# Kernel tuning notes

Hardware: AMD Instinct MI355X
Metric: run time of the kernel (lower is better)

The kernel has to match this reference:

```python
import jax, jax.numpy as jnp
import numpy as np

BINS = 10          # init kwarg `bins`
LOSS_WEIGHT = 1.0  # init kwarg `loss_weight`


def setup_inputs() -> dict:
    key = jax.random.key(0)
    k1, k2, k3 = jax.random.split(key, 3)
    B, C = 131072, 80  # [batch_num(anchors), class_num]
    pred = jax.random.normal(k1, (B, C), dtype=jnp.float32)
    target = jax.random.randint(k2, (B, C), 0, 2).astype(jnp.int32)
    label_weight = jax.random.randint(k3, (B, C), 0, 2).astype(jnp.int32)
    return {"pred": pred, "target": target, "label_weight": label_weight}


def _ghmc_loss(pred, target_f, valid_f):
    # total number of valid samples (>=1), matches max(valid.sum().item(), 1.0)
    total = jnp.maximum(valid_f.sum(), 1.0)

    # gradient magnitude g = |sigmoid(pred).detach() - target|, in [0, 1]
    g = jnp.abs(jax.nn.sigmoid(jax.lax.stop_gradient(pred)) - target_f)

    # bin index: edges are i/bins, last edge padded by 1e-6, so
    # floor(g * bins) clipped to [0, bins-1] reproduces the torch loop's
    # per-element assignment (elements exactly on an edge take the later bin,
    # matching the sequential overwrite of weights[inds]).
    bin_idx = jnp.clip(jnp.floor(g * BINS).astype(jnp.int32), 0, BINS - 1)

    # histogram of valid elements per bin (invalid routed to extra bin BINS)
    flat_idx = jnp.where(valid_f > 0, bin_idx, BINS).reshape(-1)
    counts = jnp.bincount(flat_idx, length=BINS + 1)[:BINS].astype(pred.dtype)

    # n = number of non-empty bins (>=1 whenever any element is valid)
    n = jnp.maximum((counts > 0).sum(), 1).astype(pred.dtype)

    # per-bin weight total/num_in_bin, zero for empty bins, then /n
    w_bin = jnp.where(counts > 0, total / jnp.maximum(counts, 1.0), 0.0) / n
    weights = jnp.where(valid_f > 0, w_bin[bin_idx], 0.0)
    weights = jax.lax.stop_gradient(weights)  # histogram weights are detached

    # weighted BCE-with-logits, reduction='sum', then / total
    bce = target_f * jax.nn.softplus(-pred) + (1.0 - target_f) * jax.nn.softplus(pred)
    return (weights * bce).sum() / total * LOSS_WEIGHT


def reference(pred, target, label_weight):
    target_f = target.astype(pred.dtype)
    valid_f = (label_weight > 0).astype(pred.dtype)
    return _ghmc_loss(pred, target_f, valid_f)
```

## Files before the change

### kernel.cpp

```cpp
#include <hip/hip_runtime.h>

#define BINS 10
#define TPB  256
#define NB_MAX 2048
#define FTPB 1024
#define KPACK 16384.0f
#define LN2f  0.69314718055994531f

__global__ __launch_bounds__(TPB, 4) void ghmc_hist_kernel(
    const float4* __restrict__ pred4,
    const int4*   __restrict__ tgt4,
    const int4*   __restrict__ lw4,
    float* __restrict__ part,
    int n4, int n)
{
    float acc[BINS];
#pragma unroll
    for (int b = 0; b < BINS; ++b) acc[b] = 0.f;

    auto proc = [&](float p, int t, int w) {
        float q     = __int_as_float(__float_as_int(p) ^ (t << 31));
        float e     = __builtin_amdgcn_exp2f(fabsf(q) * -1.44269504089f);
        float d     = 1.f + e;
        float r     = __builtin_amdgcn_rcpf(d);
        float num   = (q >= 0.f) ? 1.0f : e;
        float sig10 = num * (10.f * r);
        int bin     = (int)sig10;
        bin = bin < (BINS - 1) ? bin : (BINS - 1);
        float bce2  = fmaf(fmaxf(q, 0.f), 1.44269504089f,
                           __builtin_amdgcn_logf(d));
        int   vm    = 0 - (int)(w > 0);
        float v     = bce2 + KPACK;
        int   vbits = __float_as_int(v) & vm;
        int   bit   = 1 << bin;
#pragma unroll
        for (int b = 0; b < BINS; ++b) {
            int sel = __builtin_amdgcn_sbfe(bit, b, 1);
            acc[b] += __int_as_float(sel & vbits);
        }
    };

    const int tid    = threadIdx.x;
    const int stride = gridDim.x * TPB;
    const int base   = blockIdx.x * TPB + tid;
    const int full   = n4 / stride;

    int i = base;
    float4 pA; int4 tA, wA;
    if (full > 0) { pA = pred4[i]; tA = tgt4[i]; wA = lw4[i]; }
    for (int k = 0; k < full - 1; ++k) {
        const int j = i + stride;
        float4 pB = pred4[j]; int4 tB = tgt4[j]; int4 wB = lw4[j];
        proc(pA.x, tA.x, wA.x); proc(pA.y, tA.y, wA.y);
        proc(pA.z, tA.z, wA.z); proc(pA.w, tA.w, wA.w);
        pA = pB; tA = tB; wA = wB;
        i = j;
    }
    if (full > 0) {
        proc(pA.x, tA.x, wA.x); proc(pA.y, tA.y, wA.y);
        proc(pA.z, tA.z, wA.z); proc(pA.w, tA.w, wA.w);
    }
    {
        const int j = base + full * stride;
        if (j < n4) {
            float4 p = pred4[j]; int4 t = tgt4[j]; int4 w = lw4[j];
            proc(p.x, t.x, w.x); proc(p.y, t.y, w.y);
            proc(p.z, t.z, w.z); proc(p.w, t.w, w.w);
        }
    }
    if (blockIdx.x == 0 && tid < (n & 3)) {
        const float* predf = (const float*)pred4;
        const int*   tgtf  = (const int*)tgt4;
        const int*   lwf   = (const int*)lw4;
        const int j = n4 * 4 + tid;
        proc(predf[j], tgtf[j], lwf[j]);
    }

#pragma unroll
    for (int b = 0; b < BINS; ++b) {
#pragma unroll
        for (int off = 1; off <= 8; off <<= 1)
            acc[b] += __shfl_xor(acc[b], off, 64);
    }

    __shared__ float red[2 * BINS][16];
    const int grp = tid >> 4;
    if ((tid & 15) == 0) {
#pragma unroll
        for (int b = 0; b < BINS; ++b) {
            float Cf = floorf(acc[b] * (1.f / KPACK));
            red[b][grp]        = acc[b] - KPACK * Cf;
            red[BINS + b][grp] = Cf;
        }
    }
    __syncthreads();
    if (tid < 2 * BINS) {
        float v = 0.f;
#pragma unroll
        for (int g = 0; g < 16; ++g) v += red[tid][g];
        part[blockIdx.x * (2 * BINS) + tid] = v;
    }
}

__global__ __launch_bounds__(FTPB) void ghmc_final_kernel(
    const float* __restrict__ part, float* __restrict__ out, int nb)
{
    float acc[2 * BINS];
#pragma unroll
    for (int v = 0; v < 2 * BINS; ++v) acc[v] = 0.f;

    const int tid = threadIdx.x;
    for (int i = tid; i < nb; i += FTPB) {
        const float4* rec = (const float4*)(part + (size_t)i * (2 * BINS));
        float4 a = rec[0], b = rec[1], c = rec[2], d = rec[3], e = rec[4];
        acc[0]  += a.x; acc[1]  += a.y; acc[2]  += a.z; acc[3]  += a.w;
        acc[4]  += b.x; acc[5]  += b.y; acc[6]  += b.z; acc[7]  += b.w;
        acc[8]  += c.x; acc[9]  += c.y; acc[10] += c.z; acc[11] += c.w;
        acc[12] += d.x; acc[13] += d.y; acc[14] += d.z; acc[15] += d.w;
        acc[16] += e.x; acc[17] += e.y; acc[18] += e.z; acc[19] += e.w;
    }

#pragma unroll
    for (int v = 0; v < 2 * BINS; ++v) {
#pragma unroll
        for (int off = 1; off <= 32; off <<= 1)
            acc[v] += __shfl_xor(acc[v], off, 64);
    }

    __shared__ float sh[2 * BINS][16];
    const int wv = tid >> 6, lane = tid & 63;
    if (lane == 0) {
#pragma unroll
        for (int v = 0; v < 2 * BINS; ++v) sh[v][wv] = acc[v];
    }
    __syncthreads();
    if (tid < 2 * BINS) {
        float s = 0.f;
#pragma unroll
        for (int g = 0; g < 16; ++g) s += sh[tid][g];
        sh[tid][0] = s;
    }
    __syncthreads();

    if (tid == 0) {
        float ti = 0.f; int nbn = 0;
        float cnts[BINS];
#pragma unroll
        for (int b = 0; b < BINS; ++b) {
            cnts[b] = sh[BINS + b][0];
            ti += cnts[b];
            nbn += (cnts[b] > 0.f) ? 1 : 0;
        }
        float total = fmaxf(ti, 1.f);
        float nf    = (float)(nbn > 0 ? nbn : 1);
        float loss  = 0.f;
#pragma unroll
        for (int b = 0; b < BINS; ++b) {
            if (cnts[b] > 0.f) {
                float w = (total / cnts[b]) / nf;
                loss += w * (sh[b][0] * LN2f);
            }
        }
        out[0] = loss / total * 1.0f;
    }
}

extern "C" void kernel_launch(void* const* d_in, const int* in_sizes, int n_in,
                              void* d_out, int out_size, void* d_ws, size_t ws_size,
                              hipStream_t stream)
{
    const float4* pred4 = (const float4*)d_in[0];
    const int4*   tgt4  = (const int4*)d_in[1];
    const int4*   lw4   = (const int4*)d_in[2];

    const int n  = in_sizes[0];
    const int n4 = n / 4;

    int nb = (n4 + TPB - 1) / TPB;
    if (nb > NB_MAX) nb = NB_MAX;
    int ws_cap = (int)(ws_size / (2 * BINS * sizeof(float)));
    if (nb > ws_cap) nb = ws_cap;
    if (nb < 1) nb = 1;

    float* part = (float*)d_ws;

    ghmc_hist_kernel<<<nb, TPB, 0, stream>>>(pred4, tgt4, lw4, part, n4, n);
    ghmc_final_kernel<<<1, FTPB, 0, stream>>>(part, (float*)d_out, nb);
}
```

Before: 37.77 us.

## Stage inputs via async global-to-LDS double buffer and use logit-threshold cumulative bins

The input stream is now prefetched with global_load_lds into a two-slot LDS buffer, with explicit vmcnt waits, so the next tile's loads overlap compute on the current tile. Bin assignment no longer uses a sigmoid, rcp and one-hot bit extraction. Each element is compared against logit thresholds and added into cumulative bin accumulators, and the final kernel recovers per-bin counts and sums by differencing. This trades the rcp and bit select for 9 compare-selects, adds LDS traffic and hand-written waitcnt scheduling, and risks small mismatches at bin edges plus precision loss from subtracting cumulative sums.

```diff
diff --git a/kernel.cpp b/kernel.cpp
--- a/kernel.cpp
+++ b/kernel.cpp
@@ -5,7 +5,15 @@
 #define NB_MAX 2048
 #define FTPB 1024
 #define KPACK 16384.0f
-#define LN2f  0.69314718055994531f
+#define LN2f   0.69314718055994531f
+#define LOG2Ef 1.44269504088896f
+
+template <typename T>
+__device__ __forceinline__ void gload16(const T* g, T* l) {
+    __builtin_amdgcn_global_load_lds(
+        (const __attribute__((address_space(1))) void*)g,
+        (__attribute__((address_space(3))) void*)l, 16, 0, 0);
+}
 
 __global__ __launch_bounds__(TPB, 4) void ghmc_hist_kernel(
     const float4* __restrict__ pred4,
@@ -14,30 +22,30 @@
     float* __restrict__ part,
     int n4, int n)
 {
-    float acc[BINS];
-#pragma unroll
-    for (int b = 0; b < BINS; ++b) acc[b] = 0.f;
+    __shared__ float4 Lp[2][TPB];
+    __shared__ int4   Lt[2][TPB];
+    __shared__ int4   Lw[2][TPB];
+    __shared__ float  red[2 * BINS][16];
+
+    float A[BINS];
+#pragma unroll
+    for (int b = 0; b < BINS; ++b) A[b] = 0.f;
+
+    const float Q[9] = {-2.19722458f, -1.38629436f, -0.84729786f,
+                        -0.40546511f,  0.0f,         0.40546511f,
+                         0.84729786f,  1.38629436f,  2.19722458f};
 
     auto proc = [&](float p, int t, int w) {
-        float q     = __int_as_float(__float_as_int(p) ^ (t << 31));
-        float e     = __builtin_amdgcn_exp2f(fabsf(q) * -1.44269504089f);
-        float d     = 1.f + e;
-        float r     = __builtin_amdgcn_rcpf(d);
-        float num   = (q >= 0.f) ? 1.0f : e;
-        float sig10 = num * (10.f * r);
-        int bin     = (int)sig10;
-        bin = bin < (BINS - 1) ? bin : (BINS - 1);
-        float bce2  = fmaf(fmaxf(q, 0.f), 1.44269504089f,
-                           __builtin_amdgcn_logf(d));
-        int   vm    = 0 - (int)(w > 0);
-        float v     = bce2 + KPACK;
-        int   vbits = __float_as_int(v) & vm;
-        int   bit   = 1 << bin;
-#pragma unroll
-        for (int b = 0; b < BINS; ++b) {
-            int sel = __builtin_amdgcn_sbfe(bit, b, 1);
-            acc[b] += __int_as_float(sel & vbits);
-        }
+        float q    = __int_as_float(__float_as_int(p) ^ (int)((unsigned)t << 31));
+        float e    = __builtin_amdgcn_exp2f(fabsf(q) * -LOG2Ef);
+        float d    = 1.f + e;
+        float bce2 = fmaf(fmaxf(q, 0.f), LOG2Ef,
+                          __builtin_amdgcn_logf(d));
+        float v    = (w > 0) ? (bce2 + KPACK) : 0.f;
+        A[0] += v;
+#pragma unroll
+        for (int k = 0; k < 9; ++k)
+            A[k + 1] += (q >= Q[k]) ? v : 0.f;
     };
 
     const int tid    = threadIdx.x;
@@ -45,20 +53,49 @@
     const int base   = blockIdx.x * TPB + tid;
     const int full   = n4 / stride;
 
-    int i = base;
-    float4 pA; int4 tA, wA;
-    if (full > 0) { pA = pred4[i]; tA = tgt4[i]; wA = lw4[i]; }
-    for (int k = 0; k < full - 1; ++k) {
-        const int j = i + stride;
-        float4 pB = pred4[j]; int4 tB = tgt4[j]; int4 wB = lw4[j];
-        proc(pA.x, tA.x, wA.x); proc(pA.y, tA.y, wA.y);
-        proc(pA.z, tA.z, wA.z); proc(pA.w, tA.w, wA.w);
-        pA = pB; tA = tB; wA = wB;
-        i = j;
-    }
-    if (full > 0) {
-        proc(pA.x, tA.x, wA.x); proc(pA.y, tA.y, wA.y);
-        proc(pA.z, tA.z, wA.z); proc(pA.w, tA.w, wA.w);
+    if (full >= 2) {
+        gload16(&pred4[base],          &Lp[0][tid]);
+        gload16(&tgt4 [base],          &Lt[0][tid]);
+        gload16(&lw4  [base],          &Lw[0][tid]);
+        gload16(&pred4[base + stride], &Lp[1][tid]);
+        gload16(&tgt4 [base + stride], &Lt[1][tid]);
+        gload16(&lw4  [base + stride], &Lw[1][tid]);
+
+        for (int k = 0; k < full - 1; ++k) {
+            asm volatile("s_waitcnt vmcnt(3)" ::: "memory");
+            __builtin_amdgcn_sched_barrier(0);
+            const int b2 = k & 1;
+            float4 p = Lp[b2][tid];
+            int4   t = Lt[b2][tid];
+            int4   w = Lw[b2][tid];
+            asm volatile("s_waitcnt lgkmcnt(0)" ::: "memory");
+            __builtin_amdgcn_sched_barrier(0);
+            if (k + 2 < full) {
+                const int j = base + (k + 2) * stride;
+                gload16(&pred4[j], &Lp[b2][tid]);
+                gload16(&tgt4 [j], &Lt[b2][tid]);
+                gload16(&lw4  [j], &Lw[b2][tid]);
+            }
+            proc(p.x, t.x, w.x); proc(p.y, t.y, w.y);
+            proc(p.z, t.z, w.z); proc(p.w, t.w, w.w);
+        }
+        {
+            asm volatile("s_waitcnt vmcnt(0)" ::: "memory");
+            __builtin_amdgcn_sched_barrier(0);
+            const int b2 = (full - 1) & 1;
+            float4 p = Lp[b2][tid];
+            int4   t = Lt[b2][tid];
+            int4   w = Lw[b2][tid];
+            proc(p.x, t.x, w.x); proc(p.y, t.y, w.y);
+            proc(p.z, t.z, w.z); proc(p.w, t.w, w.w);
+        }
+    } else {
+        for (int k = 0; k < full; ++k) {
+            const int j = base + k * stride;
+            float4 p = pred4[j]; int4 t = tgt4[j]; int4 w = lw4[j];
+            proc(p.x, t.x, w.x); proc(p.y, t.y, w.y);
+            proc(p.z, t.z, w.z); proc(p.w, t.w, w.w);
+        }
     }
     {
         const int j = base + full * stride;
@@ -80,16 +117,15 @@
     for (int b = 0; b < BINS; ++b) {
 #pragma unroll
         for (int off = 1; off <= 8; off <<= 1)
-            acc[b] += __shfl_xor(acc[b], off, 64);
-    }
-
-    __shared__ float red[2 * BINS][16];
+            A[b] += __shfl_xor(A[b], off, 64);
+    }
+
     const int grp = tid >> 4;
     if ((tid & 15) == 0) {
 #pragma unroll
         for (int b = 0; b < BINS; ++b) {
-            float Cf = floorf(acc[b] * (1.f / KPACK));
-            red[b][grp]        = acc[b] - KPACK * Cf;
+            float Cf = floorf(A[b] * (1.f / KPACK));
+            red[b][grp]        = A[b] - KPACK * Cf;
             red[BINS + b][grp] = Cf;
         }
     }
@@ -143,22 +179,28 @@
     __syncthreads();
 
     if (tid == 0) {
-        float ti = 0.f; int nbn = 0;
-        float cnts[BINS];
+        float PS2[BINS + 1], PC[BINS + 1];
+        PS2[BINS] = 0.f; PC[BINS] = 0.f;
+#pragma unroll
+        for (int b = 0; b < BINS; ++b) { PS2[b] = sh[b][0]; PC[b] = sh[BINS + b][0]; }
+
+        float ti = PC[0];
+        int nbn = 0;
+        float cnts[BINS], sums[BINS];
 #pragma unroll
         for (int b = 0; b < BINS; ++b) {
-            cnts[b] = sh[BINS + b][0];
-            ti += cnts[b];
-            nbn += (cnts[b] > 0.f) ? 1 : 0;
+            cnts[b] = PC[b]  - PC[b + 1];
+            sums[b] = PS2[b] - PS2[b + 1];
+            nbn += (cnts[b] > 0.5f) ? 1 : 0;
         }
         float total = fmaxf(ti, 1.f);
         float nf    = (float)(nbn > 0 ? nbn : 1);
         float loss  = 0.f;
 #pragma unroll
         for (int b = 0; b < BINS; ++b) {
-            if (cnts[b] > 0.f) {
+            if (cnts[b] > 0.5f) {
                 float w = (total / cnts[b]) / nf;
-                loss += w * (sh[b][0] * LN2f);
+                loss += w * (sums[b] * LN2f);
             }
         }
         out[0] = loss / total * 1.0f;
```

After: 36.00 us. 4.7% less time.
